# Performance work log

Hardware: AMD Instinct MI355X
Metric: run time of the kernel (lower is better)

## Reference

```python
import jax, jax.numpy as jnp
import numpy as np

B, N, M, K = 2, 16384, 16384, 32
C_IN, C_OUT, KS = 64, 128, 15
RADIUS = 0.1
SIGMA = 0.5 * RADIUS  # module sets self.sigma = sigma * radius


def _generate_kernel_points(num_kpoints: int, radius: float) -> np.ndarray:
    # Fibonacci-sphere placement, matching the torch generate_kernel_points
    if num_kpoints == 1:
        return np.zeros((1, 3), dtype=np.float32)
    pts = np.zeros((num_kpoints, 3), dtype=np.float32)
    golden_angle = np.pi * (3 - np.sqrt(5))
    for i in range(num_kpoints):
        y = 1 - i / float(num_kpoints - 1) * 2
        r_y = np.sqrt(1 - y * y)
        theta = golden_angle * i
        pts[i] = np.array([np.cos(theta) * r_y, y, np.sin(theta) * r_y]) * radius
    return pts


def setup_inputs() -> dict:
    key = jax.random.key(0)
    k1, k2, k3, k4 = jax.random.split(key, 4)
    query_points = jax.random.uniform(k1, (B, N, 3), dtype=jnp.float32)
    support_points = jax.random.uniform(k2, (B, M, 3), dtype=jnp.float32)
    support_features = jax.random.normal(k3, (B, M, C_IN), dtype=jnp.float32)
    neighbor_idx = jax.random.randint(k4, (B, N, K), 0, M)
    kernel_points = jnp.asarray(_generate_kernel_points(KS, RADIUS * 0.8))
    k5 = jax.random.fold_in(key, 5)
    # kaiming-uniform-ish init on flattened (KS*C_IN, C_OUT)
    bound = np.sqrt(1.0 / (KS * C_IN))
    weights = jax.random.uniform(k5, (KS, C_IN, C_OUT), dtype=jnp.float32,
                                 minval=-bound, maxval=bound)
    bias = jnp.zeros((C_OUT,), dtype=jnp.float32)
    return {
        "query_points": query_points,
        "support_points": support_points,
        "support_features": support_features,
        "neighbor_idx": neighbor_idx,
        "kernel_points": kernel_points,
        "weights": weights,
        "bias": bias,
    }


def reference(query_points, support_points, support_features, neighbor_idx,
              kernel_points, weights, bias):
    # Batched gather: support[b, idx[b]] -> [B, N, K, *]
    gather = jax.vmap(lambda feats, idx: feats[idx])
    neighbor_points = gather(support_points, neighbor_idx)      # [B,N,K,3]
    neighbor_features = gather(support_features, neighbor_idx)  # [B,N,K,C_in]

    rel = neighbor_points - query_points[:, :, None, :]          # [B,N,K,3]
    # squared distance to each kernel point: [B,N,K,J]
    sq_dist = jnp.sum((rel[:, :, :, None, :] - kernel_points[None, None, None]) ** 2,
                      axis=-1)
    influences = jnp.exp(-sq_dist / (2 * SIGMA ** 2))
    influences = influences / (influences.sum(axis=-1, keepdims=True) + 1e-6)

    out = jnp.einsum('bnkc,bnkj,jco->bno', neighbor_features, influences, weights)
    return out + bias
```

## Files before the change

kernel.cpp:

```cpp
#include <hip/hip_runtime.h>
#include <hip/hip_bf16.h>


#define NB   16384
#define MB   16384
#define KN   32
#define CIN  64
#define COUT 128
#define KS   15
#define TP   32
#define PROW 2064
#define WF_BYTES  245760u
#define FP_BYTES  (2u * MB * CIN * 2u)
#define SP4_BYTES (2u * MB * 16u)

typedef __attribute__((ext_vector_type(8))) short short8;
typedef __attribute__((ext_vector_type(4))) float f32x4;

static __device__ __forceinline__ unsigned int pack2_bf16(float f0, float f1) {
    const unsigned int a = __float_as_uint(f0) + 0x8000u;
    const unsigned int b = __float_as_uint(f1) + 0x8000u;
    return (a >> 16) | (b & 0xffff0000u);
}

static __device__ __forceinline__ unsigned int pack2_bf16_rne(float f0, float f1) {
    unsigned int a = __float_as_uint(f0);
    unsigned int b = __float_as_uint(f1);
    a += 0x7fffu + ((a >> 16) & 1u);
    b += 0x7fffu + ((b >> 16) & 1u);
    return (a >> 16) | (b & 0xffff0000u);
}

static __device__ __forceinline__ unsigned short f32_to_bf16_rne(float x) {
    unsigned int u = __float_as_uint(x);
    u += 0x7fffu + ((u >> 16) & 1u);
    return (unsigned short)(u >> 16);
}

__global__ __launch_bounds__(256)
void prep_kernel(const float* __restrict__ Wg, const float* __restrict__ feats,
                 const float* __restrict__ sp,
                 unsigned short* __restrict__ wf, unsigned int* __restrict__ fp,
                 float4* __restrict__ sp4, int full) {
    const int bid = blockIdx.x;
    if (bid < 60) {
        const int tid = bid * 256 + threadIdx.x;
        const int l = tid & 63;
        const int t = (tid >> 6) & 7;
        const int s = tid >> 9;
        const int n  = t * 16 + (l & 15);
        const int kb = s * 32 + (l >> 4) * 8;
        short8 o;
        #pragma unroll
        for (int i = 0; i < 8; ++i)
            o[i] = (short)f32_to_bf16_rne(Wg[(kb + i) * COUT + n]);
        *(short8*)(wf + (size_t)tid * 8) = o;
    } else if (!full) {
        return;
    } else if (bid < 60 + 128) {
        const int m = (bid - 60) * 256 + threadIdx.x;
        const float* s3 = sp + 3 * (size_t)m;
        sp4[m] = make_float4(s3[0], s3[1], s3[2], 0.0f);
    } else {
        const unsigned int t = (unsigned int)(bid - 188) * 256u + threadIdx.x;
        if (t < 2u * MB * 32u) {
            const int m   = t >> 5;
            const int p2  = t & 31;
            const int n16 = p2 >> 1;
            const int tt  = (p2 & 1) * 2;
            const float a = feats[(size_t)m * CIN + tt * 16 + n16];
            const float b = feats[(size_t)m * CIN + (tt + 1) * 16 + n16];
            fp[t] = pack2_bf16_rne(a, b);
        }
    }
}

template<bool PK>
__global__ __launch_bounds__(512, 4)
void kpconv_mfma(const float* __restrict__ qp,
                 const float* __restrict__ sp,
                 const float* __restrict__ feats,
                 const unsigned int* __restrict__ fpk,
                 const float4* __restrict__ sp4,
                 const int* __restrict__ nidx,
                 const float* __restrict__ kp,
                 const unsigned short* __restrict__ wfrag,
                 const float* __restrict__ bias,
                 float* __restrict__ out) {
    __shared__ __align__(16) char sF[TP * PROW];

    const int tid  = threadIdx.x;
    const int lane = tid & 63;
    const int wv   = tid >> 6;
    const int gp_base = blockIdx.x * TP;
    const int b = gp_base >> 14;
    const float*        fbf  = feats + (size_t)b * MB * CIN;
    const unsigned int* fpb  = fpk + (size_t)b * MB * 32;
    const float4*       sp4b = sp4 + (size_t)b * MB;
    const float*        spb  = sp + (size_t)b * MB * 3;

    const int n16  = lane & 15;
    const int quad = lane >> 4;

    const int jc = n16 < 14 ? n16 : 14;
    const float kxj = kp[3 * jc + 0];
    const float kyj = kp[3 * jc + 1];
    const float kzj = kp[3 * jc + 2];

    const int gp0 = gp_base + wv * 4;
    const int* ip = nidx + (size_t)gp0 * KN + quad * 8;
    int4 nx0 = *(const int4*)(ip);
    int4 nx1 = *(const int4*)(ip + 4);

    #pragma unroll 1
    for (int pt = 0; pt < 4; ++pt) {
        const int pl = wv * 4 + pt;
        const int gp = gp0 + pt;

        int idxv[8];
        *(int4*)(&idxv[0]) = nx0;
        *(int4*)(&idxv[4]) = nx1;
        if (pt < 3) {
            const int* ipn = ip + (pt + 1) * KN;
            nx0 = *(const int4*)(ipn);
            nx1 = *(const int4*)(ipn + 4);
        }

        const float qx = qp[3 * gp + 0];
        const float qy = qp[3 * gp + 1];
        const float qz = qp[3 * gp + 2];
        const float qkx = qx + kxj, qky = qy + kyj, qkz = qz + kzj;

        float e[8];
        uint2 g[8];
        if (PK) {
            float4 s4[8];
            #pragma unroll
            for (int i = 0; i < 8; ++i) s4[i] = sp4b[idxv[i]];
            #pragma unroll
            for (int i = 0; i < 8; ++i)
                g[i] = *(const uint2*)(fpb + (size_t)idxv[i] * 32 + n16 * 2);
            #pragma unroll
            for (int i = 0; i < 8; ++i) {
                const float dx = s4[i].x - qkx;
                const float dy = s4[i].y - qky;
                const float dz = s4[i].z - qkz;
                const float d2 = fmaf(dx, dx, fmaf(dy, dy, dz * dz));
                const float ev = __expf(-200.0f * d2);
                e[i] = (n16 < 15) ? ev : 0.0f;
            }
        } else {
            #pragma unroll
            for (int i = 0; i < 8; ++i) {
                const float* s3 = spb + (size_t)idxv[i] * 3;
                const float dx = s3[0] - qkx;
                const float dy = s3[1] - qky;
                const float dz = s3[2] - qkz;
                const float d2 = fmaf(dx, dx, fmaf(dy, dy, dz * dz));
                const float ev = __expf(-200.0f * d2);
                e[i] = (n16 < 15) ? ev : 0.0f;
            }
        }

        unsigned int iu[4];
        float en[8];
        #pragma unroll
        for (int i = 0; i < 8; ++i) {
            float s = e[i];
            s += __shfl_xor(s, 1, 16);
            s += __shfl_xor(s, 2, 16);
            s += __shfl_xor(s, 4, 16);
            s += __shfl_xor(s, 8, 16);
            en[i] = e[i] * __builtin_amdgcn_rcpf(s + 1e-6f);
        }
        #pragma unroll
        for (int ih = 0; ih < 4; ++ih)
            iu[ih] = pack2_bf16(en[2 * ih], en[2 * ih + 1]);
        const short8 ifrag = *(const short8*)iu;

        unsigned int fu[4][4];
        if (PK) {
            #pragma unroll
            for (int ih = 0; ih < 4; ++ih) {
                const unsigned int ax = g[2 * ih].x, bx = g[2 * ih + 1].x;
                const unsigned int ay = g[2 * ih].y, by = g[2 * ih + 1].y;
                fu[0][ih] = __builtin_amdgcn_perm(bx, ax, 0x05040100u);
                fu[1][ih] = __builtin_amdgcn_perm(bx, ax, 0x07060302u);
                fu[2][ih] = __builtin_amdgcn_perm(by, ay, 0x05040100u);
                fu[3][ih] = __builtin_amdgcn_perm(by, ay, 0x07060302u);
            }
        } else {
            #pragma unroll
            for (int ih = 0; ih < 4; ++ih) {
                const float* fr0 = fbf + (size_t)idxv[2 * ih]     * CIN + n16;
                const float* fr1 = fbf + (size_t)idxv[2 * ih + 1] * CIN + n16;
                #pragma unroll
                for (int t = 0; t < 4; ++t)
                    fu[t][ih] = pack2_bf16(fr0[t * 16], fr1[t * 16]);
            }
        }

        #pragma unroll
        for (int t = 0; t < 4; ++t) {
            const short8 ffrag = *(const short8*)(fu[t]);
            f32x4 z = {0.f, 0.f, 0.f, 0.f};
            const f32x4 dd = __builtin_amdgcn_mfma_f32_16x16x32_bf16(ffrag, ifrag, z, 0, 0, 0);
            const unsigned int lo = pack2_bf16(dd[0], dd[1]);
            const unsigned int hi = pack2_bf16(dd[2], dd[3]);
            const int off = pl * PROW + n16 * 128 +
                            ((t * 32 + quad * 8) ^ ((n16 & 7) << 4));
            uint2 v; v.x = lo; v.y = hi;
            *(uint2*)(sF + off) = v;
        }
    }
    __syncthreads();

    const int lm = n16;
    f32x4 acc0 = {0.f, 0.f, 0.f, 0.f};
    f32x4 acc1 = {0.f, 0.f, 0.f, 0.f};
    const char* aBase = sF + lm * PROW;

    #pragma unroll
    for (int s = 0; s < 30; ++s) {
        const int j   = s >> 1;
        const int c0b = (s & 1) * 64 + quad * 16;
        const int off = j * 128 + (c0b ^ ((j & 7) << 4));
        const short8 a0 = *(const short8*)(aBase + off);
        const short8 a1 = *(const short8*)(aBase + 16 * PROW + off);
        const short8 bf = *(const short8*)(wfrag + ((size_t)(s * 8 + wv) * 64 + lane) * 8);
        acc0 = __builtin_amdgcn_mfma_f32_16x16x32_bf16(a0, bf, acc0, 0, 0, 0);
        acc1 = __builtin_amdgcn_mfma_f32_16x16x32_bf16(a1, bf, acc1, 0, 0, 0);
    }

    const float bsv = bias[wv * 16 + lm];
    #pragma unroll
    for (int r = 0; r < 4; ++r) {
        const int pr = quad * 4 + r;
        out[(size_t)(gp_base + pr)      * COUT + wv * 16 + lm] = acc0[r] + bsv;
        out[(size_t)(gp_base + 16 + pr) * COUT + wv * 16 + lm] = acc1[r] + bsv;
    }
}

extern "C" void kernel_launch(void* const* d_in, const int* in_sizes, int n_in,
                              void* d_out, int out_size, void* d_ws, size_t ws_size,
                              hipStream_t stream) {
    const float* qp = (const float*)d_in[0];
    const float* sp = (const float*)d_in[1];
    const float* ft = (const float*)d_in[2];
    const int*   ni = (const int*)d_in[3];
    const float* kp = (const float*)d_in[4];
    const float* wg = (const float*)d_in[5];
    const float* bs = (const float*)d_in[6];
    float* o = (float*)d_out;

    unsigned short* wfrag = (unsigned short*)d_ws;
    unsigned int*   fpk   = (unsigned int*)((char*)d_ws + WF_BYTES);
    float4*         sp4   = (float4*)((char*)d_ws + WF_BYTES + FP_BYTES);
    const int full = (ws_size >= (size_t)(WF_BYTES + FP_BYTES + SP4_BYTES)) ? 1 : 0;

    const int prep_blocks = full ? (60 + 128 + 4096) : 60;
    hipLaunchKernelGGL(prep_kernel, dim3(prep_blocks), dim3(256), 0, stream,
                       wg, ft, sp, wfrag, fpk, sp4, full);

    if (full) {
        hipLaunchKernelGGL((kpconv_mfma<true>), dim3((2 * NB) / TP), dim3(512), 0, stream,
                           qp, sp, ft, fpk, sp4, ni, kp, wfrag, bs, o);
    } else {
        hipLaunchKernelGGL((kpconv_mfma<false>), dim3((2 * NB) / TP), dim3(512), 0, stream,
                           qp, sp, ft, fpk, sp4, ni, kp, wfrag, bs, o);
    }
}
```

Baseline: 111.6 us.

## Use DPP row rotates for influence sums and remap GEMM wave tiling

Swaps the shuffle-xor reductions over 16 lanes for DPP row_ror adds, which avoids ds_bpermute LDS traffic. The padding lane's kernel point is placed far away so its exp underflows to zero, which removes a per-element select. The second-stage GEMM is remapped so each wave owns one 16-point M tile and two 16-column N tiles. Each wave now reuses one A fragment from LDS across two weight fragments, trading fewer LDS reads for twice as many global weight-fragment loads per wave.

```diff
diff --git a/kernel.cpp b/kernel.cpp
--- a/kernel.cpp
+++ b/kernel.cpp
@@ -16,6 +16,10 @@
 
 typedef __attribute__((ext_vector_type(8))) short short8;
 typedef __attribute__((ext_vector_type(4))) float f32x4;
+
+#define ROR_ADD(s, ctrl) \
+    ((s) + __int_as_float(__builtin_amdgcn_update_dpp( \
+        0, __float_as_int(s), (ctrl), 0xF, 0xF, true)))
 
 static __device__ __forceinline__ unsigned int pack2_bf16(float f0, float f1) {
     const unsigned int a = __float_as_uint(f0) + 0x8000u;
@@ -102,10 +106,14 @@
     const int n16  = lane & 15;
     const int quad = lane >> 4;
 
-    const int jc = n16 < 14 ? n16 : 14;
-    const float kxj = kp[3 * jc + 0];
-    const float kyj = kp[3 * jc + 1];
-    const float kzj = kp[3 * jc + 2];
+    float kxj, kyj, kzj;
+    if (n16 < 15) {
+        kxj = kp[3 * n16 + 0];
+        kyj = kp[3 * n16 + 1];
+        kzj = kp[3 * n16 + 2];
+    } else {
+        kxj = 1.0e4f; kyj = 1.0e4f; kzj = 1.0e4f;
+    }
 
     const int gp0 = gp_base + wv * 4;
     const int* ip = nidx + (size_t)gp0 * KN + quad * 8;
@@ -146,8 +154,7 @@
                 const float dy = s4[i].y - qky;
                 const float dz = s4[i].z - qkz;
                 const float d2 = fmaf(dx, dx, fmaf(dy, dy, dz * dz));
-                const float ev = __expf(-200.0f * d2);
-                e[i] = (n16 < 15) ? ev : 0.0f;
+                e[i] = __expf(-200.0f * d2);
             }
         } else {
             #pragma unroll
@@ -157,8 +164,7 @@
                 const float dy = s3[1] - qky;
                 const float dz = s3[2] - qkz;
                 const float d2 = fmaf(dx, dx, fmaf(dy, dy, dz * dz));
-                const float ev = __expf(-200.0f * d2);
-                e[i] = (n16 < 15) ? ev : 0.0f;
+                e[i] = __expf(-200.0f * d2);
             }
         }
 
@@ -167,10 +173,10 @@
         #pragma unroll
         for (int i = 0; i < 8; ++i) {
             float s = e[i];
-            s += __shfl_xor(s, 1, 16);
-            s += __shfl_xor(s, 2, 16);
-            s += __shfl_xor(s, 4, 16);
-            s += __shfl_xor(s, 8, 16);
+            s = ROR_ADD(s, 0x128);
+            s = ROR_ADD(s, 0x124);
+            s = ROR_ADD(s, 0x122);
+            s = ROR_ADD(s, 0x121);
             en[i] = e[i] * __builtin_amdgcn_rcpf(s + 1e-6f);
         }
         #pragma unroll
@@ -215,29 +221,32 @@
     }
     __syncthreads();
 
-    const int lm = n16;
+    const int mt = wv & 1;
+    const int np = wv >> 1;
+    const int t0 = np * 2, t1 = np * 2 + 1;
     f32x4 acc0 = {0.f, 0.f, 0.f, 0.f};
     f32x4 acc1 = {0.f, 0.f, 0.f, 0.f};
-    const char* aBase = sF + lm * PROW;
+    const char* aBase = sF + (size_t)(mt * 16 + n16) * PROW;
 
     #pragma unroll
     for (int s = 0; s < 30; ++s) {
         const int j   = s >> 1;
         const int c0b = (s & 1) * 64 + quad * 16;
         const int off = j * 128 + (c0b ^ ((j & 7) << 4));
-        const short8 a0 = *(const short8*)(aBase + off);
-        const short8 a1 = *(const short8*)(aBase + 16 * PROW + off);
-        const short8 bf = *(const short8*)(wfrag + ((size_t)(s * 8 + wv) * 64 + lane) * 8);
-        acc0 = __builtin_amdgcn_mfma_f32_16x16x32_bf16(a0, bf, acc0, 0, 0, 0);
-        acc1 = __builtin_amdgcn_mfma_f32_16x16x32_bf16(a1, bf, acc1, 0, 0, 0);
-    }
-
-    const float bsv = bias[wv * 16 + lm];
+        const short8 a  = *(const short8*)(aBase + off);
+        const short8 b0 = *(const short8*)(wfrag + ((size_t)(s * 8 + t0) * 64 + lane) * 8);
+        const short8 b1 = *(const short8*)(wfrag + ((size_t)(s * 8 + t1) * 64 + lane) * 8);
+        acc0 = __builtin_amdgcn_mfma_f32_16x16x32_bf16(a, b0, acc0, 0, 0, 0);
+        acc1 = __builtin_amdgcn_mfma_f32_16x16x32_bf16(a, b1, acc1, 0, 0, 0);
+    }
+
+    const float bs0 = bias[t0 * 16 + n16];
+    const float bs1 = bias[t1 * 16 + n16];
     #pragma unroll
     for (int r = 0; r < 4; ++r) {
-        const int pr = quad * 4 + r;
-        out[(size_t)(gp_base + pr)      * COUT + wv * 16 + lm] = acc0[r] + bsv;
-        out[(size_t)(gp_base + 16 + pr) * COUT + wv * 16 + lm] = acc1[r] + bsv;
+        const int pr = mt * 16 + quad * 4 + r;
+        out[(size_t)(gp_base + pr) * COUT + t0 * 16 + n16] = acc0[r] + bs0;
+        out[(size_t)(gp_base + pr) * COUT + t1 * 16 + n16] = acc1[r] + bs1;
     }
 }
 
```

After: 115.7 us. 1.04x slower.
